# Performance work log

Measured on AMD Instinct MI355X. Metric: run time of the kernel, lower is better.

Reference implementation:

```python
import jax, jax.numpy as jnp
import numpy as np

B, T, I, H, L = 128, 512, 512, 1024, 2
KEEP = 0.9  # 1 - dropout_rate


def setup_inputs() -> dict:
    key = jax.random.key(0)
    ks = jax.random.split(key, 13)
    s = 0.02
    bern = lambda k, shape: (jax.random.bernoulli(k, KEEP, shape) / KEEP).astype(jnp.float32)
    return {
        "x": jax.random.normal(ks[0], (B, T, I), dtype=jnp.float32),
        "W_ih0": jax.random.normal(ks[1], (4 * H, I), dtype=jnp.float32) * s,
        "W_hh0": jax.random.normal(ks[2], (4 * H, H), dtype=jnp.float32) * s,
        "b_ih0": jax.random.normal(ks[3], (4 * H,), dtype=jnp.float32) * s,
        "b_hh0": jax.random.normal(ks[4], (4 * H,), dtype=jnp.float32) * s,
        "W_ih1": jax.random.normal(ks[5], (4 * H, H), dtype=jnp.float32) * s,
        "W_hh1": jax.random.normal(ks[6], (4 * H, H), dtype=jnp.float32) * s,
        "b_ih1": jax.random.normal(ks[7], (4 * H,), dtype=jnp.float32) * s,
        "b_hh1": jax.random.normal(ks[8], (4 * H,), dtype=jnp.float32) * s,
        "out_mask": bern(ks[9], (L, B, H)),
        "h_mask": bern(ks[10], (L, B, H)),
        "c_mask": bern(ks[11], (L, B, H)),
    }


def _run_layer(x_tbi, W_ih, W_hh, b_ih, b_hh, om, hm, cm):
    """x_tbi: [T,B,in]; masks: [B,H]. Returns ([T,B,H] outputs, final (h,c))."""
    h0 = jnp.zeros((x_tbi.shape[1], H), dtype=x_tbi.dtype)
    c0 = jnp.zeros_like(h0)
    # precompute input projections for all timesteps: [T,B,4H]
    xg = jnp.einsum('tbi,gi->tbg', x_tbi, W_ih) + b_ih + b_hh

    def step(carry, xg_t):
        h, c = carry
        gates = xg_t + h @ W_hh.T  # [B,4H]
        i, f, g, o = jnp.split(gates, 4, axis=-1)
        i, f, o = jax.nn.sigmoid(i), jax.nn.sigmoid(f), jax.nn.sigmoid(o)
        g = jnp.tanh(g)
        c2 = f * c + i * g
        h2 = o * jnp.tanh(c2)
        out = h2 * om
        return (h2 * hm, c2 * cm), out

    (hf, cf), ys = jax.lax.scan(step, (h0, c0), xg)
    return ys, (hf, cf)


def reference(x, W_ih0, W_hh0, b_ih0, b_hh0, W_ih1, W_hh1, b_ih1, b_hh1,
              out_mask, h_mask, c_mask):
    layers = [(W_ih0, W_hh0, b_ih0, b_hh0), (W_ih1, W_hh1, b_ih1, b_hh1)]
    xt = jnp.transpose(x, (1, 0, 2))  # [T,B,I]
    for l, (Wi, Wh, bi, bh) in enumerate(layers):
        xt, (hf, cf) = _run_layer(xt, Wi, Wh, bi, bh,
                                  out_mask[l], h_mask[l], c_mask[l])
    out = jnp.transpose(xt, (1, 0, 2))  # [B,T,H]
    return out, (hf[None], cf[None])
```

## Files before the change

### kernel.cpp

```cpp
#include <hip/hip_runtime.h>

#define B_  128
#define T_  512
#define I_  512
#define H_  1024
#define G4  4096
#define SLOT 262144L

typedef __attribute__((ext_vector_type(8))) short   short8;
typedef __attribute__((ext_vector_type(4))) short   short4v;
typedef __attribute__((ext_vector_type(4))) float   f32x4;
typedef unsigned long long u64;

__device__ __forceinline__ float bf2f(short u){
  return __uint_as_float(((unsigned)(unsigned short)u) << 16);
}
__device__ __forceinline__ short f2bf(float f){
  unsigned u = __float_as_uint(f);
  unsigned r = (u + 0x7FFFu + ((u >> 16) & 1u)) >> 16;
  return (short)r;
}
__device__ __forceinline__ float sigm(float x){ return 1.0f/(1.0f + __expf(-x)); }
__device__ __forceinline__ float tanh_(float x){ return 1.0f - 2.0f/(__expf(2.0f*x) + 1.0f); }

__global__ __launch_bounds__(256) void cvt_bf16(const float* __restrict__ in,
                                                short* __restrict__ out, int nq){
  int i = blockIdx.x*256 + threadIdx.x;
  if (i >= nq) return;
  float4 v = ((const float4*)in)[i];
  short4v o; o.x = f2bf(v.x); o.y = f2bf(v.y); o.z = f2bf(v.z); o.w = f2bf(v.w);
  ((short4v*)out)[i] = o;
}

__global__ __launch_bounds__(256) void swz_whh(const float* __restrict__ W,
                                               short* __restrict__ out){
  int c = blockIdx.x*256 + threadIdx.x;
  int l = c & 63, ks = (c >> 6) & 31, wvv = (c >> 11) & 7, jb = c >> 14;
  int g = wvv >> 1, ct = wvv & 1;
  long row = (long)(g*1024 + jb*32 + ct*16 + (l & 15));
  int col = ks*32 + (l >> 4)*8;
  const float* src = W + row*H_ + col;
  short8 o;
#pragma unroll
  for (int e = 0; e < 8; ++e) o[e] = f2bf(src[e]);
  ((short8*)out)[c] = o;
}

template<int K>
__global__ __launch_bounds__(256) void proj_gemm(const short* __restrict__ A,
                                                 const short* __restrict__ W,
                                                 const float* __restrict__ bih,
                                                 const float* __restrict__ bhh,
                                                 short* __restrict__ C){
  __shared__ short lds[2][2][128*40];
  const int tid = threadIdx.x;
  const int l  = tid & 63, wv = tid >> 6;
  const int wm = wv >> 1,  wn = wv & 1;
  const int nt = blockIdx.x, mt = blockIdx.y;
  const int r0 = tid >> 2, cb = (tid & 3) * 8;
  const short* Ab = A + (long)(mt*128 + r0)*K + cb;
  const short* Wb = W + (long)(nt*128 + r0)*K + cb;
  const int lo  = r0*40 + cb;
  const int lo2 = lo + 64*40;
  const int NK = K/32;

  short8 pa0 = *(const short8*)(Ab);
  short8 pa1 = *(const short8*)(Ab + 64*K);
  short8 pb0 = *(const short8*)(Wb);
  short8 pb1 = *(const short8*)(Wb + 64*K);
  *(short8*)&lds[0][0][lo]  = pa0;
  *(short8*)&lds[0][0][lo2] = pa1;
  *(short8*)&lds[0][1][lo]  = pb0;
  *(short8*)&lds[0][1][lo2] = pb1;

  f32x4 acc[4][4];
  f32x4 z = {0.f,0.f,0.f,0.f};
#pragma unroll
  for (int i = 0; i < 4; ++i)
#pragma unroll
    for (int j = 0; j < 4; ++j) acc[i][j] = z;

  for (int kt = 0; kt < NK; ++kt){
    __syncthreads();
    if (kt + 1 < NK){
      pa0 = *(const short8*)(Ab + (kt+1)*32);
      pa1 = *(const short8*)(Ab + (kt+1)*32 + 64*K);
      pb0 = *(const short8*)(Wb + (kt+1)*32);
      pb1 = *(const short8*)(Wb + (kt+1)*32 + 64*K);
    }
    const short* As = lds[kt & 1][0];
    const short* Bs = lds[kt & 1][1];
    short8 bfr[4];
#pragma unroll
    for (int nf = 0; nf < 4; ++nf)
      bfr[nf] = *(const short8*)&Bs[(wn*64 + nf*16 + (l & 15))*40 + (l >> 4)*8];
#pragma unroll
    for (int mf = 0; mf < 4; ++mf){
      short8 af = *(const short8*)&As[(wm*64 + mf*16 + (l & 15))*40 + (l >> 4)*8];
#pragma unroll
      for (int nf = 0; nf < 4; ++nf)
        acc[mf][nf] = __builtin_amdgcn_mfma_f32_16x16x32_bf16(af, bfr[nf], acc[mf][nf], 0, 0, 0);
    }
    if (kt + 1 < NK){
      int nb = (kt + 1) & 1;
      *(short8*)&lds[nb][0][lo]  = pa0;
      *(short8*)&lds[nb][0][lo2] = pa1;
      *(short8*)&lds[nb][1][lo]  = pb0;
      *(short8*)&lds[nb][1][lo2] = pb1;
    }
  }

  const int mrow0 = mt*128 + wm*64;
  const int ncol0 = nt*128 + wn*64;
#pragma unroll
  for (int nf = 0; nf < 4; ++nf){
    int n = ncol0 + nf*16 + (l & 15);
    int g   = n >> 10;
    int jb  = (n & 1023) >> 5;
    int jl5 = n & 31;
    float bs = bih[n] + bhh[n];
#pragma unroll
    for (int mf = 0; mf < 4; ++mf){
#pragma unroll
      for (int r = 0; r < 4; ++r){
        int m = mrow0 + mf*16 + (l >> 4)*4 + r;
        int b = m >> 9, t = m & 511;
        long idx = ((((long)t*8 + (b >> 4))*32 + jb)*4 + g)*512 + (b & 15)*32 + jl5;
        C[idx] = f2bf(acc[mf][nf][r] + bs);
      }
    }
  }
}

template<int LAYER, bool RING>
__global__ __launch_bounds__(512, 2) void lstm_scan(
    short* __restrict__ hring, const short* __restrict__ Wsw, const short* __restrict__ xg,
    const float* __restrict__ om, const float* __restrict__ hm, const float* __restrict__ cm,
    short* __restrict__ out0, float* __restrict__ dout,
    int* __restrict__ flags)
{
  const int tid = threadIdx.x;
  const int l = tid & 63, wv = tid >> 6;
  const int bt = blockIdx.x, jb = blockIdx.y;

  short8 w[32];
  {
    const short8* wp = (const short8*)Wsw + ((long)(jb*8 + wv)*32)*64 + l;
#pragma unroll
    for (int ks = 0; ks < 32; ++ks) w[ks] = wp[ks*64];
    f32x4* wf = (f32x4*)w;
#pragma unroll
    for (int i = 0; i < 32; ++i) asm volatile("" : "+v"(wf[i]));
  }

  const int bl = tid >> 5, jl = tid & 31;
  const int jcol = jb*32 + jl;
  const long bj = (long)(bt*16 + bl)*H_ + jcol;
  const float mo = om[bj], mh = hm[bj], mc = cm[bj];
  float c = 0.f;
  const int rr = bl & 3;
  const int l2 = (jl & 15) + ((bl >> 2) << 4);
  const int sidx = (bl + ((jl >> 3) << 4))*8 + (jl & 7);

  __shared__ __align__(16) short hbuf[2048*8];
  __shared__ float red[8*264];
  __shared__ __align__(16) short sstage[512];
  int* flbase = flags + (long)bt*T_*32;

  const short* xg0 = xg + (((long)bt)*32 + jb)*2048;
  short xv0 = xg0[tid], xv1 = xg0[512 + tid], xv2 = xg0[1024 + tid], xv3 = xg0[1536 + tid];

  for (int t = 0; t < T_; ++t){
    const long slotoff  = RING ? (long)t*SLOT     : (long)(t & 1)*SLOT;
    const long nslotoff = RING ? (long)(t+1)*SLOT : (long)((t+1) & 1)*SLOT;

    {
      const char* hsl = (const char*)hring + slotoff + (long)bt*32768;
#pragma unroll
      for (int i = 0; i < 4; ++i){
        int ci = wv*256 + i*64 + l;
        short8 v;
        if constexpr (RING){
          v = *(const short8*)(hsl + (long)ci*16);
        } else {
          const u64* ap = (const u64*)(hsl + (long)ci*16);
          union { u64 q[2]; short8 s; } uu;
          uu.q[0] = __hip_atomic_load(ap,     __ATOMIC_RELAXED, __HIP_MEMORY_SCOPE_AGENT);
          uu.q[1] = __hip_atomic_load(ap + 1, __ATOMIC_RELAXED, __HIP_MEMORY_SCOPE_AGENT);
          v = uu.s;
        }
        *(short8*)&hbuf[ci*8] = v;
      }
    }
    __syncthreads();

    f32x4 acc0 = {0.f,0.f,0.f,0.f}, acc1 = {0.f,0.f,0.f,0.f};
#pragma unroll
    for (int kb = 0; kb < 4; ++kb){
      short8 aa[8];
#pragma unroll
      for (int k8 = 0; k8 < 8; ++k8)
        aa[k8] = *(const short8*)&hbuf[((kb*8 + k8)*64 + l)*8];
#pragma unroll
      for (int k8 = 0; k8 < 8; ++k8){
        if (k8 & 1) acc1 = __builtin_amdgcn_mfma_f32_16x16x32_bf16(aa[k8], w[kb*8 + k8], acc1, 0, 0, 0);
        else        acc0 = __builtin_amdgcn_mfma_f32_16x16x32_bf16(aa[k8], w[kb*8 + k8], acc0, 0, 0, 0);
      }
    }
    f32x4 accs;
#pragma unroll
    for (int r = 0; r < 4; ++r) accs[r] = acc0[r] + acc1[r];

    *(f32x4*)&red[wv*264 + l*4] = accs;
    __syncthreads();

    float gate[4];
    short xvv[4] = {xv0, xv1, xv2, xv3};
#pragma unroll
    for (int g = 0; g < 4; ++g){
      int wvg = g*2 + (jl >> 4);
      gate[g] = red[wvg*264 + l2*4 + rr] + bf2f(xvv[g]);
    }
    float ii = sigm(gate[0]);
    float ff = sigm(gate[1]);
    float gg = tanh_(gate[2]);
    float oo = sigm(gate[3]);
    float c2 = ff*c + ii*gg;
    float h2 = oo*tanh_(c2);
    c = c2*mc;
    float hn = h2*mh;

    if (t == T_ - 1){
      if (LAYER == 0){
        out0[((long)(bt*16 + bl)*T_ + t)*H_ + jcol] = f2bf(h2*mo);
      } else {
        dout[((long)(bt*16 + bl)*T_ + t)*H_ + jcol] = h2*mo;
        dout[(long)B_*T_*H_ + bj] = hn;
        dout[(long)B_*T_*H_ + (long)B_*H_ + bj] = c;
      }
      break;
    }

    sstage[sidx] = f2bf(hn);
    __syncthreads();

    if (wv == 0){
      short8 pk = ((const short8*)sstage)[l];
      char* hdst = (char*)hring + nslotoff + ((long)bt*2048 + jb*64 + l)*16;
      if constexpr (RING){
        asm volatile("global_store_dwordx4 %0, %1, off sc1" :: "v"(hdst), "v"(pk) : "memory");
      } else {
        union { short8 s; u64 q[2]; } uu; uu.s = pk;
        u64* qp = (u64*)hdst;
        __hip_atomic_store(qp,     uu.q[0], __ATOMIC_RELAXED, __HIP_MEMORY_SCOPE_AGENT);
        __hip_atomic_store(qp + 1, uu.q[1], __ATOMIC_RELAXED, __HIP_MEMORY_SCOPE_AGENT);
      }
      asm volatile("s_waitcnt vmcnt(0)" ::: "memory");
      if (tid == 0)
        __hip_atomic_store(&flbase[(long)t*32 + jb], 1, __ATOMIC_RELAXED, __HIP_MEMORY_SCOPE_AGENT);
    }

    if (LAYER == 0){
      out0[((long)(bt*16 + bl)*T_ + t)*H_ + jcol] = f2bf(h2*mo);
    } else {
      dout[((long)(bt*16 + bl)*T_ + t)*H_ + jcol] = h2*mo;
    }
    const short* xgn = xg + (((long)(t+1)*8 + bt)*32 + jb)*2048;
    xv0 = xgn[tid]; xv1 = xgn[512 + tid]; xv2 = xgn[1024 + tid]; xv3 = xgn[1536 + tid];

    {
      const u64* fp = (const u64*)&flbase[(long)t*32];
      int spins = 0;
      while (true){
        int ok = 1;
        if (l < 16){
          u64 v = __hip_atomic_load(fp + l, __ATOMIC_RELAXED, __HIP_MEMORY_SCOPE_AGENT);
          ok = ((unsigned)v != 0u) & ((unsigned)(v >> 32) != 0u);
        }
        if (__all(ok)) break;
        if (++spins > (1 << 18)) break;
        if (spins > 4) __builtin_amdgcn_s_sleep(1);
      }
    }
    __builtin_amdgcn_fence(__ATOMIC_ACQUIRE, "workgroup");
  }
}

extern "C" void kernel_launch(void* const* d_in, const int* in_sizes, int n_in,
                              void* d_out, int out_size, void* d_ws, size_t ws_size,
                              hipStream_t stream){
  const float* x    = (const float*)d_in[0];
  const float* Wih0 = (const float*)d_in[1];
  const float* Whh0 = (const float*)d_in[2];
  const float* bih0 = (const float*)d_in[3];
  const float* bhh0 = (const float*)d_in[4];
  const float* Wih1 = (const float*)d_in[5];
  const float* Whh1 = (const float*)d_in[6];
  const float* bih1 = (const float*)d_in[7];
  const float* bhh1 = (const float*)d_in[8];
  const float* omsk = (const float*)d_in[9];
  const float* hmsk = (const float*)d_in[10];
  const float* cmsk = (const float*)d_in[11];
  float* out = (float*)d_out;

  char* p = (char*)d_ws;
  auto alloc = [&](size_t bytes)->char*{
    char* r = p; p += (bytes + 255) & ~(size_t)255; return r;
  };
  short* xg      = (short*)alloc((size_t)65536*4096*2);
  short* out0_bf = (short*)alloc((size_t)67108864*2);
  short* x_bf    = (short*)out0_bf;
  short* wih0_bf = (short*)alloc((size_t)2097152*2);
  short* wih1_bf = (short*)alloc((size_t)4194304*2);
  short* whh0_sw = (short*)alloc((size_t)4194304*2);
  short* whh1_sw = (short*)alloc((size_t)4194304*2);
  int*   flags0  = (int*)alloc((size_t)8*512*32*4);
  int*   flags1  = (int*)alloc((size_t)8*512*32*4);
  size_t fixed = (size_t)(p - (char*)d_ws);
  bool ring = (fixed + (size_t)512*SLOT) <= ws_size;
  short* hring = (short*)alloc(ring ? (size_t)512*SLOT : (size_t)2*SLOT);
  if ((size_t)(p - (char*)d_ws) > ws_size) return;

  hipMemsetAsync(flags0, 0, (size_t)8*512*32*4, stream);
  hipMemsetAsync(flags1, 0, (size_t)8*512*32*4, stream);
  hipMemsetAsync(hring, 0, (size_t)SLOT, stream);

  cvt_bf16<<<33554432/4/256, 256, 0, stream>>>(x,    x_bf,    33554432/4);
  cvt_bf16<<<2097152/4/256,  256, 0, stream>>>(Wih0, wih0_bf, 2097152/4);
  cvt_bf16<<<4194304/4/256,  256, 0, stream>>>(Wih1, wih1_bf, 4194304/4);
  swz_whh <<<524288/256,     256, 0, stream>>>(Whh0, whh0_sw);
  swz_whh <<<524288/256,     256, 0, stream>>>(Whh1, whh1_sw);

  proj_gemm<512><<<dim3(32, 512), 256, 0, stream>>>(x_bf, wih0_bf, bih0, bhh0, xg);
  if (ring)
    lstm_scan<0, true ><<<dim3(8, 32), 512, 0, stream>>>(hring, whh0_sw, xg,
        omsk, hmsk, cmsk, out0_bf, nullptr, flags0);
  else
    lstm_scan<0, false><<<dim3(8, 32), 512, 0, stream>>>(hring, whh0_sw, xg,
        omsk, hmsk, cmsk, out0_bf, nullptr, flags0);

  proj_gemm<1024><<<dim3(32, 512), 256, 0, stream>>>(out0_bf, wih1_bf, bih1, bhh1, xg);
  if (ring)
    lstm_scan<1, true ><<<dim3(8, 32), 512, 0, stream>>>(hring, whh1_sw, xg,
        omsk + 131072, hmsk + 131072, cmsk + 131072, nullptr, out, flags1);
  else
    lstm_scan<1, false><<<dim3(8, 32), 512, 0, stream>>>(hring, whh1_sw, xg,
        omsk + 131072, hmsk + 131072, cmsk + 131072, nullptr, out, flags1);
}
```

Baseline: 4.513 ms.

## Split recurrent matvec by K-halves, load h directly to registers, skip t=0 GEMM

The LSTM scan kernel now has each wave own two column tiles over half of K, loading h directly from global into registers instead of staging all of h through LDS with a barrier. Partial sums from the two K-halves are combined in the gate stage. The h publish path drops one LDS barrier, spreads stores across all waves, and pads the flags to one every 16 bytes. It also skips the recurrent GEMM at t=0 so the h ring no longer needs zeroing. The projection output layout and weight swizzle change to match the new thread-to-element mapping. The cost is a larger reduction buffer and more global loads per wave.

New measurement: 6.420 ms. +42.3%, slower.

```diff
diff --git a/kernel.cpp b/kernel.cpp
--- a/kernel.cpp
+++ b/kernel.cpp
@@ -35,10 +35,10 @@
 __global__ __launch_bounds__(256) void swz_whh(const float* __restrict__ W,
                                                short* __restrict__ out){
   int c = blockIdx.x*256 + threadIdx.x;
-  int l = c & 63, ks = (c >> 6) & 31, wvv = (c >> 11) & 7, jb = c >> 14;
-  int g = wvv >> 1, ct = wvv & 1;
+  int l = c & 63, ks = (c >> 6) & 15, ct = (c >> 10) & 1, wvv = (c >> 11) & 7, jb = c >> 14;
+  int g = wvv >> 1, kh = wvv & 1;
   long row = (long)(g*1024 + jb*32 + ct*16 + (l & 15));
-  int col = ks*32 + (l >> 4)*8;
+  int col = kh*512 + ks*32 + (l >> 4)*8;
   const float* src = W + row*H_ + col;
   short8 o;
 #pragma unroll
@@ -125,8 +125,10 @@
       for (int r = 0; r < 4; ++r){
         int m = mrow0 + mf*16 + (l >> 4)*4 + r;
         int b = m >> 9, t = m & 511;
-        long idx = ((((long)t*8 + (b >> 4))*32 + jb)*4 + g)*512 + (b & 15)*32 + jl5;
-        C[idx] = f2bf(acc[mf][nf][r] + bs);
+        int idx2 = (jl5 >> 3)*16 + (b & 15);
+        int pos  = (idx2 >> 3)*64 + (idx2 & 7)*8 + (jl5 & 7);
+        long o = ((((long)t*8 + (b >> 4))*32 + jb)*4 + g)*512 + pos;
+        C[o] = f2bf(acc[mf][nf][r] + bs);
       }
     }
   }
@@ -134,7 +136,8 @@
 
 template<int LAYER, bool RING>
 __global__ __launch_bounds__(512, 2) void lstm_scan(
-    short* __restrict__ hring, const short* __restrict__ Wsw, const short* __restrict__ xg,
+    short* __restrict__ hring,
+    const short* __restrict__ Wsw, const short* __restrict__ xg,
     const float* __restrict__ om, const float* __restrict__ hm, const float* __restrict__ cm,
     short* __restrict__ out0, float* __restrict__ dout,
     int* __restrict__ flags)
@@ -143,29 +146,33 @@
   const int l = tid & 63, wv = tid >> 6;
   const int bt = blockIdx.x, jb = blockIdx.y;
 
-  short8 w[32];
+  short8 w0[16], w1[16];
   {
-    const short8* wp = (const short8*)Wsw + ((long)(jb*8 + wv)*32)*64 + l;
-#pragma unroll
-    for (int ks = 0; ks < 32; ++ks) w[ks] = wp[ks*64];
-    f32x4* wf = (f32x4*)w;
-#pragma unroll
-    for (int i = 0; i < 32; ++i) asm volatile("" : "+v"(wf[i]));
+    const short8* wp = (const short8*)Wsw + ((long)((jb*8 + wv)*2)*16)*64 + l;
+#pragma unroll
+    for (int ks = 0; ks < 16; ++ks) w0[ks] = wp[ks*64];
+#pragma unroll
+    for (int ks = 0; ks < 16; ++ks) w1[ks] = wp[(16 + ks)*64];
+    f32x4* wf0 = (f32x4*)w0;
+    f32x4* wf1 = (f32x4*)w1;
+#pragma unroll
+    for (int i = 0; i < 16; ++i){ asm volatile("" : "+v"(wf0[i])); asm volatile("" : "+v"(wf1[i])); }
   }
 
-  const int bl = tid >> 5, jl = tid & 31;
+  const int idx = wv*8 + (l >> 3);
+  const int bl  = idx & 15;
+  const int jl  = ((idx >> 4) << 3) + (l & 7);
   const int jcol = jb*32 + jl;
   const long bj = (long)(bt*16 + bl)*H_ + jcol;
   const float mo = om[bj], mh = hm[bj], mc = cm[bj];
   float c = 0.f;
+  const int ct_r = jl >> 4;
+  const int lane_src = (jl & 15) + ((bl >> 2) << 4);
   const int rr = bl & 3;
-  const int l2 = (jl & 15) + ((bl >> 2) << 4);
-  const int sidx = (bl + ((jl >> 3) << 4))*8 + (jl & 7);
-
-  __shared__ __align__(16) short hbuf[2048*8];
-  __shared__ float red[8*264];
+
+  __shared__ float red[16*264];
   __shared__ __align__(16) short sstage[512];
-  int* flbase = flags + (long)bt*T_*32;
+  int* flbase = flags + (long)bt*T_*128;
 
   const short* xg0 = xg + (((long)bt)*32 + jb)*2048;
   short xv0 = xg0[tid], xv1 = xg0[512 + tid], xv2 = xg0[1024 + tid], xv3 = xg0[1536 + tid];
@@ -174,52 +181,55 @@
     const long slotoff  = RING ? (long)t*SLOT     : (long)(t & 1)*SLOT;
     const long nslotoff = RING ? (long)(t+1)*SLOT : (long)((t+1) & 1)*SLOT;
 
-    {
-      const char* hsl = (const char*)hring + slotoff + (long)bt*32768;
-#pragma unroll
-      for (int i = 0; i < 4; ++i){
-        int ci = wv*256 + i*64 + l;
-        short8 v;
-        if constexpr (RING){
-          v = *(const short8*)(hsl + (long)ci*16);
-        } else {
-          const u64* ap = (const u64*)(hsl + (long)ci*16);
+    if (t > 0){
+      const char* hsl = (const char*)hring + slotoff + (long)bt*32768
+                      + (long)(((wv & 1)*16)*64 + l)*16;
+      short8 a[16];
+      if constexpr (RING){
+#pragma unroll
+        for (int ks = 0; ks < 16; ++ks)
+          a[ks] = *(const short8*)(hsl + (long)ks*1024);
+      } else {
+#pragma unroll
+        for (int ks = 0; ks < 16; ++ks){
+          const u64* ap = (const u64*)(hsl + (long)ks*1024);
           union { u64 q[2]; short8 s; } uu;
           uu.q[0] = __hip_atomic_load(ap,     __ATOMIC_RELAXED, __HIP_MEMORY_SCOPE_AGENT);
           uu.q[1] = __hip_atomic_load(ap + 1, __ATOMIC_RELAXED, __HIP_MEMORY_SCOPE_AGENT);
-          v = uu.s;
+          a[ks] = uu.s;
         }
-        *(short8*)&hbuf[ci*8] = v;
-      }
-    }
-    __syncthreads();
-
-    f32x4 acc0 = {0.f,0.f,0.f,0.f}, acc1 = {0.f,0.f,0.f,0.f};
-#pragma unroll
-    for (int kb = 0; kb < 4; ++kb){
-      short8 aa[8];
-#pragma unroll
-      for (int k8 = 0; k8 < 8; ++k8)
-        aa[k8] = *(const short8*)&hbuf[((kb*8 + k8)*64 + l)*8];
-#pragma unroll
-      for (int k8 = 0; k8 < 8; ++k8){
-        if (k8 & 1) acc1 = __builtin_amdgcn_mfma_f32_16x16x32_bf16(aa[k8], w[kb*8 + k8], acc1, 0, 0, 0);
-        else        acc0 = __builtin_amdgcn_mfma_f32_16x16x32_bf16(aa[k8], w[kb*8 + k8], acc0, 0, 0, 0);
-      }
-    }
-    f32x4 accs;
-#pragma unroll
-    for (int r = 0; r < 4; ++r) accs[r] = acc0[r] + acc1[r];
-
-    *(f32x4*)&red[wv*264 + l*4] = accs;
-    __syncthreads();
+      }
+
+      f32x4 a00 = {0.f,0.f,0.f,0.f}, a01 = {0.f,0.f,0.f,0.f};
+      f32x4 a10 = {0.f,0.f,0.f,0.f}, a11 = {0.f,0.f,0.f,0.f};
+#pragma unroll
+      for (int ks = 0; ks < 16; ++ks){
+        if (ks & 1){
+          a01 = __builtin_amdgcn_mfma_f32_16x16x32_bf16(a[ks], w0[ks], a01, 0, 0, 0);
+          a11 = __builtin_amdgcn_mfma_f32_16x16x32_bf16(a[ks], w1[ks], a11, 0, 0, 0);
+        } else {
+          a00 = __builtin_amdgcn_mfma_f32_16x16x32_bf16(a[ks], w0[ks], a00, 0, 0, 0);
+          a10 = __builtin_amdgcn_mfma_f32_16x16x32_bf16(a[ks], w1[ks], a10, 0, 0, 0);
+        }
+      }
+      f32x4 s0, s1;
+#pragma unroll
+      for (int r = 0; r < 4; ++r){ s0[r] = a00[r] + a01[r]; s1[r] = a10[r] + a11[r]; }
+      *(f32x4*)&red[(wv*2 + 0)*264 + l*4] = s0;
+      *(f32x4*)&red[(wv*2 + 1)*264 + l*4] = s1;
+      __syncthreads();
+    }
 
     float gate[4];
     short xvv[4] = {xv0, xv1, xv2, xv3};
 #pragma unroll
     for (int g = 0; g < 4; ++g){
-      int wvg = g*2 + (jl >> 4);
-      gate[g] = red[wvg*264 + l2*4 + rr] + bf2f(xvv[g]);
+      float rv = 0.f;
+      if (t > 0){
+        rv = red[((g*2 + 0)*2 + ct_r)*264 + lane_src*4 + rr]
+           + red[((g*2 + 1)*2 + ct_r)*264 + lane_src*4 + rr];
+      }
+      gate[g] = rv + bf2f(xvv[g]);
     }
     float ii = sigm(gate[0]);
     float ff = sigm(gate[1]);
@@ -241,12 +251,13 @@
       break;
     }
 
-    sstage[sidx] = f2bf(hn);
-    __syncthreads();
-
-    if (wv == 0){
-      short8 pk = ((const short8*)sstage)[l];
-      char* hdst = (char*)hring + nslotoff + ((long)bt*2048 + jb*64 + l)*16;
+    sstage[wv*64 + l] = f2bf(hn);
+    asm volatile("s_waitcnt lgkmcnt(0)" ::: "memory");
+    __builtin_amdgcn_sched_barrier(0);
+    if (l < 8){
+      short8 pk = *(const short8*)&sstage[wv*64 + l*8];
+      char* hdst = (char*)hring + nslotoff
+                 + ((long)bt*2048 + jb*64 + wv*8 + l)*16;
       if constexpr (RING){
         asm volatile("global_store_dwordx4 %0, %1, off sc1" :: "v"(hdst), "v"(pk) : "memory");
       } else {
@@ -255,10 +266,12 @@
         __hip_atomic_store(qp,     uu.q[0], __ATOMIC_RELAXED, __HIP_MEMORY_SCOPE_AGENT);
         __hip_atomic_store(qp + 1, uu.q[1], __ATOMIC_RELAXED, __HIP_MEMORY_SCOPE_AGENT);
       }
-      asm volatile("s_waitcnt vmcnt(0)" ::: "memory");
-      if (tid == 0)
-        __hip_atomic_store(&flbase[(long)t*32 + jb], 1, __ATOMIC_RELAXED, __HIP_MEMORY_SCOPE_AGENT);
-    }
+    }
+    asm volatile("s_waitcnt vmcnt(0)" ::: "memory");
+    __syncthreads();
+    if (tid == 0)
+      __hip_atomic_store(&flbase[((long)t*32 + jb)*4], 1,
+                         __ATOMIC_RELAXED, __HIP_MEMORY_SCOPE_AGENT);
 
     if (LAYER == 0){
       out0[((long)(bt*16 + bl)*T_ + t)*H_ + jcol] = f2bf(h2*mo);
@@ -269,19 +282,18 @@
     xv0 = xgn[tid]; xv1 = xgn[512 + tid]; xv2 = xgn[1024 + tid]; xv3 = xgn[1536 + tid];
 
     {
-      const u64* fp = (const u64*)&flbase[(long)t*32];
+      const int* fp = &flbase[(long)t*128];
       int spins = 0;
       while (true){
-        int ok = 1;
-        if (l < 16){
-          u64 v = __hip_atomic_load(fp + l, __ATOMIC_RELAXED, __HIP_MEMORY_SCOPE_AGENT);
-          ok = ((unsigned)v != 0u) & ((unsigned)(v >> 32) != 0u);
-        }
-        if (__all(ok)) break;
+        int v = 1;
+        if (l < 32)
+          v = __hip_atomic_load(fp + l*4, __ATOMIC_RELAXED, __HIP_MEMORY_SCOPE_AGENT);
+        if (__all(v != 0)) break;
         if (++spins > (1 << 18)) break;
         if (spins > 4) __builtin_amdgcn_s_sleep(1);
       }
     }
+    __builtin_amdgcn_sched_barrier(0);
     __builtin_amdgcn_fence(__ATOMIC_ACQUIRE, "workgroup");
   }
 }
@@ -314,16 +326,15 @@
   short* wih1_bf = (short*)alloc((size_t)4194304*2);
   short* whh0_sw = (short*)alloc((size_t)4194304*2);
   short* whh1_sw = (short*)alloc((size_t)4194304*2);
-  int*   flags0  = (int*)alloc((size_t)8*512*32*4);
-  int*   flags1  = (int*)alloc((size_t)8*512*32*4);
+  int*   flags0  = (int*)alloc((size_t)8*512*32*4*4);
+  int*   flags1  = (int*)alloc((size_t)8*512*32*4*4);
   size_t fixed = (size_t)(p - (char*)d_ws);
   bool ring = (fixed + (size_t)512*SLOT) <= ws_size;
   short* hring = (short*)alloc(ring ? (size_t)512*SLOT : (size_t)2*SLOT);
   if ((size_t)(p - (char*)d_ws) > ws_size) return;
 
-  hipMemsetAsync(flags0, 0, (size_t)8*512*32*4, stream);
-  hipMemsetAsync(flags1, 0, (size_t)8*512*32*4, stream);
-  hipMemsetAsync(hring, 0, (size_t)SLOT, stream);
+  hipMemsetAsync(flags0, 0, (size_t)8*512*32*4*4, stream);
+  hipMemsetAsync(flags1, 0, (size_t)8*512*32*4*4, stream);
 
   cvt_bf16<<<33554432/4/256, 256, 0, stream>>>(x,    x_bf,    33554432/4);
   cvt_bf16<<<2097152/4/256,  256, 0, stream>>>(Wih0, wih0_bf, 2097152/4);
```
